# Kernel optimization log

Measured on AMD Instinct MI355X. Metric: run time of the kernel, lower is better.

The kernel has to match this reference:

```python
import jax, jax.numpy as jnp
import numpy as np

B, L, D, A = 64, 512, 512, 512  # batch, seq_len, word_embed_size, alignment_size


def setup_inputs() -> dict:
    key = jax.random.key(0)
    k1, k2, k3 = jax.random.split(key, 3)
    premises = jax.random.normal(k1, (B, L, D), dtype=jnp.float32)
    hypotheses = jax.random.normal(k2, (B, L, D), dtype=jnp.float32)
    W_F = jax.random.uniform(k3, (D, A), dtype=jnp.float32, minval=-1.0, maxval=1.0)
    return {"premises": premises, "hypotheses": hypotheses, "W_F": W_F}


def reference(premises, hypotheses, W_F):
    # tanh-projected cross attention (decomposable-attention align step)
    F_p = jnp.tanh(jnp.einsum('bpd,da->bpa', premises, W_F))    # [B, Lp, A]
    F_h = jnp.tanh(jnp.einsum('bhd,da->bha', hypotheses, W_F))  # [B, Lh, A]
    eijs = jnp.einsum('bpa,bha->bph', F_p, F_h)                 # [B, Lp, Lh] (unscaled)
    attn = jax.nn.softmax(eijs, axis=-1)                        # softmax over hypothesis axis
    betas = jnp.einsum('bph,bhd->bpd', attn, hypotheses)        # [B, Lp, D]
    alphas = jnp.einsum('bph,bpd->bhd', attn, premises)         # [B, Lh, D] (transpose(attn) @ P)
    return betas, alphas
```

## Files before the change

kernel.cpp:

```cpp
#include <hip/hip_runtime.h>
#include <hip/hip_fp16.h>


#define NB 64
#define NL 512
#define ND 512
#define BATCH_ELEMS (512 * 512)
#define TOT_ELEMS   ((size_t)NB * NL * ND)

typedef _Float16 h8 __attribute__((ext_vector_type(8)));
typedef float f4 __attribute__((ext_vector_type(4)));

__device__ __forceinline__ int swz(int row, int chunk) {
    return (row << 5) + ((chunk ^ (((row >> 1) ^ (row >> 4)) & 3)) << 3);
}

__device__ __forceinline__ float fast_tanh(float x) {
    float e = __expf(2.0f * x);
    return 1.0f - 2.0f / (e + 1.0f);
}

template <bool WITH_LO>
__global__ __launch_bounds__(256) void transpose_f16_kernel(
    const float* __restrict__ src, _Float16* __restrict__ dstH,
    _Float16* __restrict__ dstL)
{
    __shared__ float tile[64 * 68];
    const size_t base = (size_t)blockIdx.z * BATCH_ELEMS;
    const int r0 = blockIdx.y * 64, c0 = blockIdx.x * 64;
    const int t = threadIdx.x;
    {
        int r = t >> 2, cq = (t & 3) * 16;
        const float* sp = src + base + (size_t)(r0 + r) * 512 + c0 + cq;
        *(float4*)&tile[r * 68 + cq]      = ((const float4*)sp)[0];
        *(float4*)&tile[r * 68 + cq + 4]  = ((const float4*)sp)[1];
        *(float4*)&tile[r * 68 + cq + 8]  = ((const float4*)sp)[2];
        *(float4*)&tile[r * 68 + cq + 12] = ((const float4*)sp)[3];
    }
    __syncthreads();
    {
        int c = t >> 2, rq = (t & 3) * 16;
        _Float16 hv[16], lv[16];
#pragma unroll
        for (int j = 0; j < 16; ++j) {
            float v = tile[(rq + j) * 68 + c];
            hv[j] = (_Float16)v;
            if (WITH_LO) lv[j] = (_Float16)(v - (float)hv[j]);
        }
        _Float16* dp = dstH + base + (size_t)(c0 + c) * 512 + r0 + rq;
        *(h8*)dp = *(h8*)&hv[0];
        *(h8*)(dp + 8) = *(h8*)&hv[8];
        if (WITH_LO) {
            _Float16* dl = dstL + base + (size_t)(c0 + c) * 512 + r0 + rq;
            *(h8*)dl = *(h8*)&lv[0];
            *(h8*)(dl + 8) = *(h8*)&lv[8];
        }
    }
}

__global__ __launch_bounds__(256) void transpose_hp_kernel(
    const float* __restrict__ H, const float* __restrict__ P,
    _Float16* __restrict__ HT, _Float16* __restrict__ PT)
{
    __shared__ float tile[64 * 68];
    const int z = blockIdx.z;
    const float* src = (z < NB) ? H : P;
    _Float16* dst = (z < NB) ? HT : PT;
    const size_t base = (size_t)(z < NB ? z : z - NB) * BATCH_ELEMS;
    const int r0 = blockIdx.y * 64, c0 = blockIdx.x * 64;
    const int t = threadIdx.x;
    {
        int r = t >> 2, cq = (t & 3) * 16;
        const float* sp = src + base + (size_t)(r0 + r) * 512 + c0 + cq;
        *(float4*)&tile[r * 68 + cq]      = ((const float4*)sp)[0];
        *(float4*)&tile[r * 68 + cq + 4]  = ((const float4*)sp)[1];
        *(float4*)&tile[r * 68 + cq + 8]  = ((const float4*)sp)[2];
        *(float4*)&tile[r * 68 + cq + 12] = ((const float4*)sp)[3];
    }
    __syncthreads();
    {
        int c = t >> 2, rq = (t & 3) * 16;
        _Float16 hv[16];
#pragma unroll
        for (int j = 0; j < 16; ++j) hv[j] = (_Float16)tile[(rq + j) * 68 + c];
        _Float16* dp = dst + base + (size_t)(c0 + c) * 512 + r0 + rq;
        *(h8*)dp = *(h8*)&hv[0];
        *(h8*)(dp + 8) = *(h8*)&hv[8];
    }
}

__global__ __launch_bounds__(256) void proj_tanh_kernel(
    const float* __restrict__ P, const float* __restrict__ H,
    const _Float16* __restrict__ WTH, const _Float16* __restrict__ WTL,
    _Float16* __restrict__ Fout)
{
    __shared__ __align__(16) _Float16 AsH[2][128 * 32];
    __shared__ __align__(16) _Float16 BsH[2][128 * 32], BsL[2][128 * 32];

    const int z = blockIdx.z;
    const float* X = z ? H : P;
    _Float16* F = Fout + (size_t)z * TOT_ELEMS;
    const int r0 = blockIdx.x * 128;
    const int n0 = blockIdx.y * 128;

    const int t = threadIdx.x;
    const int lane = t & 63, w = t >> 6;
    const int q = lane >> 4, c = lane & 15;
    const int wm = w >> 1, wn = w & 1;

    f4 acc[4][4] = {};

    const int ar = t >> 1, akq = (t & 1) << 4;
    const int br = t >> 1, bcp = (t & 1) << 1;

    const float* apg = X + (size_t)(r0 + ar) * 512 + akq;
    const _Float16* bhg = WTH + (size_t)(n0 + br) * 512 + bcp * 8;
    const _Float16* blg = WTL + (size_t)(n0 + br) * 512 + bcp * 8;

    float av[2][16];
    h8 bh0[2], bh1[2], bl0[2], bl1[2];

    auto LOAD = [&](int k0, int s) {
        *(float4*)&av[s][0]  = ((const float4*)(apg + k0))[0];
        *(float4*)&av[s][4]  = ((const float4*)(apg + k0))[1];
        *(float4*)&av[s][8]  = ((const float4*)(apg + k0))[2];
        *(float4*)&av[s][12] = ((const float4*)(apg + k0))[3];
        bh0[s] = ((const h8*)(bhg + k0))[0];
        bh1[s] = ((const h8*)(bhg + k0))[1];
        bl0[s] = ((const h8*)(blg + k0))[0];
        bl1[s] = ((const h8*)(blg + k0))[1];
    };
    auto STAGE = [&](int s, int pp) {
        _Float16* asd = &AsH[pp][0];
        _Float16* bhd = &BsH[pp][0];
        _Float16* bld = &BsL[pp][0];
        const int cbase = akq >> 3;
#pragma unroll
        for (int jj = 0; jj < 2; ++jj) {
            h8 hv;
#pragma unroll
            for (int i = 0; i < 8; ++i) hv[i] = (_Float16)av[s][jj * 8 + i];
            *(h8*)&asd[swz(ar, cbase + jj)] = hv;
        }
        *(h8*)&bhd[swz(br, bcp)]     = bh0[s];
        *(h8*)&bhd[swz(br, bcp + 1)] = bh1[s];
        *(h8*)&bld[swz(br, bcp)]     = bl0[s];
        *(h8*)&bld[swz(br, bcp + 1)] = bl1[s];
    };

    LOAD(0, 0);
    STAGE(0, 0);
    LOAD(32, 1);

    for (int ks = 0; ks < 16; ++ks) {
        __syncthreads();
        const int pp = ks & 1;
        if (ks + 2 < 16) LOAD((ks + 2) << 5, pp);

        const _Float16* ash = &AsH[pp][0];
        const _Float16* bhs = &BsH[pp][0];
        const _Float16* bls = &BsL[pp][0];
        h8 aH[4], bH[4], bL[4];
#pragma unroll
        for (int mi = 0; mi < 4; ++mi)
            aH[mi] = *(const h8*)&ash[swz(wm * 64 + mi * 16 + c, q)];
#pragma unroll
        for (int ni = 0; ni < 4; ++ni) {
            bH[ni] = *(const h8*)&bhs[swz(wn * 64 + ni * 16 + c, q)];
            bL[ni] = *(const h8*)&bls[swz(wn * 64 + ni * 16 + c, q)];
        }
#pragma unroll
        for (int mi = 0; mi < 4; ++mi)
#pragma unroll
            for (int ni = 0; ni < 4; ++ni) {
                acc[mi][ni] = __builtin_amdgcn_mfma_f32_16x16x32_f16(aH[mi], bH[ni], acc[mi][ni], 0, 0, 0);
                acc[mi][ni] = __builtin_amdgcn_mfma_f32_16x16x32_f16(aH[mi], bL[ni], acc[mi][ni], 0, 0, 0);
            }
        if (ks + 1 < 16) STAGE((ks + 1) & 1, pp ^ 1);
    }

#pragma unroll
    for (int mi = 0; mi < 4; ++mi)
#pragma unroll
        for (int ni = 0; ni < 4; ++ni) {
            int col = n0 + wn * 64 + ni * 16 + c;
            int rowb = r0 + wm * 64 + mi * 16 + q * 4;
#pragma unroll
            for (int r = 0; r < 4; ++r)
                F[(size_t)(rowb + r) * 512 + col] = (_Float16)fast_tanh(acc[mi][ni][r]);
        }
}

__global__ __launch_bounds__(256) void score_softmax_kernel(
    const _Float16* __restrict__ Fbase, _Float16* __restrict__ attn)
{
    __shared__ __align__(16) _Float16 As[2][64 * 32];
    __shared__ __align__(16) _Float16 Bs[2][512 * 32];
    __shared__ float redM[4 * 64], redS[4 * 64];

    const _Float16* Fp = Fbase;
    const _Float16* Fh = Fbase + TOT_ELEMS;
    const int b = blockIdx.y;
    const int p0 = blockIdx.x * 64;
    const size_t fb = (size_t)b * BATCH_ELEMS;

    const int t = threadIdx.x, lane = t & 63, w = t >> 6;
    const int q = lane >> 4, c = lane & 15;

    f4 acc[4][8] = {};

    const int arow = t >> 2, ach = t & 3;
    const _Float16* apg = Fp + fb + (size_t)(p0 + arow) * 512 + ach * 8;
    const _Float16* bpg = Fh + fb + (size_t)(t * 2) * 512;

    h8 areg, breg[2][4];

    auto LOAD = [&](int k0) {
        areg = *(const h8*)(apg + k0);
#pragma unroll
        for (int rr = 0; rr < 2; ++rr)
#pragma unroll
            for (int ch = 0; ch < 4; ++ch)
                breg[rr][ch] = *(const h8*)(bpg + (size_t)rr * 512 + k0 + ch * 8);
    };
    auto STAGE = [&](int pp) {
        *(h8*)&As[pp][swz(arow, ach)] = areg;
#pragma unroll
        for (int rr = 0; rr < 2; ++rr)
#pragma unroll
            for (int ch = 0; ch < 4; ++ch)
                *(h8*)&Bs[pp][swz(t * 2 + rr, ch)] = breg[rr][ch];
    };

    LOAD(0);
    STAGE(0);

    int pp = 0;
    for (int k0 = 0; k0 < 512; k0 += 32) {
        __syncthreads();
        const bool more = (k0 + 32) < 512;
        if (more) LOAD(k0 + 32);

        h8 a[4], bb[8];
#pragma unroll
        for (int mt = 0; mt < 4; ++mt) a[mt] = *(const h8*)&As[pp][swz(mt * 16 + c, q)];
#pragma unroll
        for (int nt = 0; nt < 8; ++nt) bb[nt] = *(const h8*)&Bs[pp][swz(w * 128 + nt * 16 + c, q)];
#pragma unroll
        for (int mt = 0; mt < 4; ++mt)
#pragma unroll
            for (int nt = 0; nt < 8; ++nt)
                acc[mt][nt] = __builtin_amdgcn_mfma_f32_16x16x32_f16(a[mt], bb[nt], acc[mt][nt], 0, 0, 0);
        if (more) STAGE(pp ^ 1);
        pp ^= 1;
    }

    float rmax[4][4];
#pragma unroll
    for (int mt = 0; mt < 4; ++mt)
#pragma unroll
        for (int r = 0; r < 4; ++r) {
            float m = acc[mt][0][r];
#pragma unroll
            for (int nt = 1; nt < 8; ++nt) m = fmaxf(m, acc[mt][nt][r]);
            rmax[mt][r] = m;
        }
#pragma unroll
    for (int s = 1; s < 16; s <<= 1)
#pragma unroll
        for (int mt = 0; mt < 4; ++mt)
#pragma unroll
            for (int r = 0; r < 4; ++r)
                rmax[mt][r] = fmaxf(rmax[mt][r], __shfl_xor(rmax[mt][r], s, 64));
    if (c == 0)
#pragma unroll
        for (int mt = 0; mt < 4; ++mt)
#pragma unroll
            for (int r = 0; r < 4; ++r)
                redM[w * 64 + mt * 16 + q * 4 + r] = rmax[mt][r];
    __syncthreads();

    float gmax[4][4];
#pragma unroll
    for (int mt = 0; mt < 4; ++mt)
#pragma unroll
        for (int r = 0; r < 4; ++r) {
            int row = mt * 16 + q * 4 + r;
            float m = redM[row];
#pragma unroll
            for (int w4 = 1; w4 < 4; ++w4) m = fmaxf(m, redM[w4 * 64 + row]);
            gmax[mt][r] = m;
        }

    float rsum[4][4] = {};
#pragma unroll
    for (int mt = 0; mt < 4; ++mt)
#pragma unroll
        for (int nt = 0; nt < 8; ++nt)
#pragma unroll
            for (int r = 0; r < 4; ++r) {
                float e = __expf(acc[mt][nt][r] - gmax[mt][r]);
                acc[mt][nt][r] = e;
                rsum[mt][r] += e;
            }
#pragma unroll
    for (int s = 1; s < 16; s <<= 1)
#pragma unroll
        for (int mt = 0; mt < 4; ++mt)
#pragma unroll
            for (int r = 0; r < 4; ++r)
                rsum[mt][r] += __shfl_xor(rsum[mt][r], s, 64);
    if (c == 0)
#pragma unroll
        for (int mt = 0; mt < 4; ++mt)
#pragma unroll
            for (int r = 0; r < 4; ++r)
                redS[w * 64 + mt * 16 + q * 4 + r] = rsum[mt][r];
    __syncthreads();

    float inv[4][4];
#pragma unroll
    for (int mt = 0; mt < 4; ++mt)
#pragma unroll
        for (int r = 0; r < 4; ++r) {
            int row = mt * 16 + q * 4 + r;
            float s = redS[row] + redS[64 + row] + redS[128 + row] + redS[192 + row];
            inv[mt][r] = 1.0f / s;
        }

#pragma unroll
    for (int mt = 0; mt < 4; ++mt)
#pragma unroll
        for (int nt = 0; nt < 8; ++nt) {
            int col = w * 128 + nt * 16 + c;
#pragma unroll
            for (int r = 0; r < 4; ++r) {
                int row = p0 + mt * 16 + q * 4 + r;
                attn[fb + (size_t)row * 512 + col] = (_Float16)(acc[mt][nt][r] * inv[mt][r]);
            }
        }
}

__global__ __launch_bounds__(256) void out_gemm_kernel(
    const _Float16* __restrict__ Amat, const _Float16* __restrict__ HT,
    const _Float16* __restrict__ PT, float* __restrict__ out)
{
    __shared__ __align__(16) _Float16 As[2][128 * 32];
    __shared__ __align__(16) _Float16 Bs[2][128 * 32];

    const int zz = blockIdx.z;
    const bool transA = zz >= NB;
    const int b = transA ? zz - NB : zz;
    const _Float16* BT = transA ? PT : HT;
    float* Cout = transA ? out + TOT_ELEMS : out;

    const int bn = blockIdx.x * 128, bm = blockIdx.y * 128;
    const size_t base = (size_t)b * BATCH_ELEMS;

    const int t = threadIdx.x, lane = t & 63, w = t >> 6;
    const int q = lane >> 4, c = lane & 15;
    const int wm = w >> 1, wn = w & 1;

    f4 acc[4][4] = {};

    const int row2 = t >> 1, cp2 = (t & 1) * 2;
    const int kk = t >> 3, m0 = (t & 7) * 16;
    const _Float16* apg_d = Amat + base + (size_t)(bm + row2) * 512 + cp2 * 8;
    const _Float16* apg_t = Amat + base + (size_t)kk * 512 + bm + m0;
    const _Float16* bpg   = BT + base + (size_t)(bn + row2) * 512 + cp2 * 8;

    h8 a0[2], a1[2], b0[2], b1[2];

    auto LOAD = [&](int k0, int s) {
        if (!transA) {
            a0[s] = ((const h8*)(apg_d + k0))[0];
            a1[s] = ((const h8*)(apg_d + k0))[1];
        } else {
            a0[s] = ((const h8*)(apg_t + (size_t)k0 * 512))[0];
            a1[s] = ((const h8*)(apg_t + (size_t)k0 * 512))[1];
        }
        b0[s] = ((const h8*)(bpg + k0))[0];
        b1[s] = ((const h8*)(bpg + k0))[1];
    };
    auto STAGE = [&](int s, int pp) {
        if (!transA) {
            *(h8*)&As[pp][swz(row2, cp2)]     = a0[s];
            *(h8*)&As[pp][swz(row2, cp2 + 1)] = a1[s];
        } else {
#pragma unroll
            for (int j = 0; j < 8; ++j) {
                As[pp][swz(m0 + j, kk >> 3) + (kk & 7)]     = a0[s][j];
                As[pp][swz(m0 + 8 + j, kk >> 3) + (kk & 7)] = a1[s][j];
            }
        }
        *(h8*)&Bs[pp][swz(row2, cp2)]     = b0[s];
        *(h8*)&Bs[pp][swz(row2, cp2 + 1)] = b1[s];
    };

    LOAD(0, 0);
    STAGE(0, 0);
    LOAD(32, 1);

    for (int ks = 0; ks < 16; ++ks) {
        __syncthreads();
        const int pp = ks & 1;
        if (ks + 2 < 16) LOAD((ks + 2) << 5, pp);

        h8 a[4], bb[4];
#pragma unroll
        for (int mi = 0; mi < 4; ++mi) a[mi] = *(const h8*)&As[pp][swz(wm * 64 + mi * 16 + c, q)];
#pragma unroll
        for (int ni = 0; ni < 4; ++ni) bb[ni] = *(const h8*)&Bs[pp][swz(wn * 64 + ni * 16 + c, q)];
#pragma unroll
        for (int mi = 0; mi < 4; ++mi)
#pragma unroll
            for (int ni = 0; ni < 4; ++ni)
                acc[mi][ni] = __builtin_amdgcn_mfma_f32_16x16x32_f16(a[mi], bb[ni], acc[mi][ni], 0, 0, 0);
        if (ks + 1 < 16) STAGE((ks + 1) & 1, pp ^ 1);
    }

#pragma unroll
    for (int mi = 0; mi < 4; ++mi)
#pragma unroll
        for (int ni = 0; ni < 4; ++ni) {
            int col = bn + wn * 64 + ni * 16 + c;
            int rowb = bm + wm * 64 + mi * 16 + q * 4;
#pragma unroll
            for (int r = 0; r < 4; ++r)
                Cout[base + (size_t)(rowb + r) * 512 + col] = acc[mi][ni][r];
        }
}

extern "C" void kernel_launch(void* const* d_in, const int* in_sizes, int n_in,
                              void* d_out, int out_size, void* d_ws, size_t ws_size,
                              hipStream_t stream) {
    const float* P = (const float*)d_in[0];
    const float* H = (const float*)d_in[1];
    const float* W = (const float*)d_in[2];
    float* out = (float*)d_out;

    _Float16* ws16 = (_Float16*)d_ws;
    _Float16* F    = ws16;
    _Float16* PT   = ws16;
    _Float16* HT   = ws16 + TOT_ELEMS;
    _Float16* attn = ws16 + 2 * TOT_ELEMS;
    _Float16* WTH  = attn;
    _Float16* WTL  = attn + BATCH_ELEMS;

    transpose_f16_kernel<true><<<dim3(8, 8, 1), 256, 0, stream>>>(W, WTH, WTL);
    proj_tanh_kernel<<<dim3(256, 4, 2), 256, 0, stream>>>(P, H, WTH, WTL, F);
    score_softmax_kernel<<<dim3(8, NB), 256, 0, stream>>>(F, attn);
    transpose_hp_kernel<<<dim3(8, 8, 2 * NB), 256, 0, stream>>>(H, P, HT, PT);
    out_gemm_kernel<<<dim3(4, 4, 2 * NB), 256, 0, stream>>>(attn, HT, PT, out);
}
```

Before: 506.9 us.

## Use direct global-to-LDS loads in GEMM kernels and pre-convert inputs to fp16

Replaces the register-staged double-buffer loads in the projection, score and output GEMM kernels with global_load_lds direct-to-LDS copies. The swizzle is applied on the source address so the existing LDS layout is kept. To make the projection input fp16 for these loads, a new conversion kernel writes P and H as fp16 into the output buffer as scratch before the main pipeline. The aim is to cut VGPR staging and LDS write instructions. The cost is an extra pass over the inputs and a different synchronisation pattern per k-step.

Result: no change. 503.9 us (-0.6%).

```diff
diff --git a/kernel.cpp b/kernel.cpp
--- a/kernel.cpp
+++ b/kernel.cpp
@@ -15,9 +15,33 @@
     return (row << 5) + ((chunk ^ (((row >> 1) ^ (row >> 4)) & 3)) << 3);
 }
 
+__device__ __forceinline__ void gld16(const _Float16* g, _Float16* l) {
+    __builtin_amdgcn_global_load_lds(
+        (const __attribute__((address_space(1))) void*)g,
+        (__attribute__((address_space(3))) void*)l, 16, 0, 0);
+}
+
 __device__ __forceinline__ float fast_tanh(float x) {
     float e = __expf(2.0f * x);
     return 1.0f - 2.0f / (e + 1.0f);
+}
+
+__global__ __launch_bounds__(256) void conv16_kernel(
+    const float* __restrict__ P, const float* __restrict__ H,
+    _Float16* __restrict__ X16)
+{
+    const int z = blockIdx.z;
+    const float* src = z ? H : P;
+    _Float16* dst = X16 + (size_t)z * TOT_ELEMS;
+    size_t i = ((size_t)blockIdx.x * 256 + threadIdx.x) * 8;
+    float4 v0 = ((const float4*)(src + i))[0];
+    float4 v1 = ((const float4*)(src + i))[1];
+    h8 o;
+    o[0] = (_Float16)v0.x; o[1] = (_Float16)v0.y;
+    o[2] = (_Float16)v0.z; o[3] = (_Float16)v0.w;
+    o[4] = (_Float16)v1.x; o[5] = (_Float16)v1.y;
+    o[6] = (_Float16)v1.z; o[7] = (_Float16)v1.w;
+    *(h8*)(dst + i) = o;
 }
 
 template <bool WITH_LO>
@@ -90,7 +114,7 @@
 }
 
 __global__ __launch_bounds__(256) void proj_tanh_kernel(
-    const float* __restrict__ P, const float* __restrict__ H,
+    const _Float16* __restrict__ X16,
     const _Float16* __restrict__ WTH, const _Float16* __restrict__ WTL,
     _Float16* __restrict__ Fout)
 {
@@ -98,76 +122,53 @@
     __shared__ __align__(16) _Float16 BsH[2][128 * 32], BsL[2][128 * 32];
 
     const int z = blockIdx.z;
-    const float* X = z ? H : P;
+    const _Float16* X = X16 + (size_t)z * TOT_ELEMS;
     _Float16* F = Fout + (size_t)z * TOT_ELEMS;
     const int r0 = blockIdx.x * 128;
     const int n0 = blockIdx.y * 128;
 
     const int t = threadIdx.x;
-    const int lane = t & 63, w = t >> 6;
+    const int lane = t & 63, w4 = t >> 6;
     const int q = lane >> 4, c = lane & 15;
-    const int wm = w >> 1, wn = w & 1;
+    const int wm = w4 >> 1, wn = w4 & 1;
 
     f4 acc[4][4] = {};
 
-    const int ar = t >> 1, akq = (t & 1) << 4;
-    const int br = t >> 1, bcp = (t & 1) << 1;
-
-    const float* apg = X + (size_t)(r0 + ar) * 512 + akq;
-    const _Float16* bhg = WTH + (size_t)(n0 + br) * 512 + bcp * 8;
-    const _Float16* blg = WTL + (size_t)(n0 + br) * 512 + bcp * 8;
-
-    float av[2][16];
-    h8 bh0[2], bh1[2], bl0[2], bl1[2];
-
-    auto LOAD = [&](int k0, int s) {
-        *(float4*)&av[s][0]  = ((const float4*)(apg + k0))[0];
-        *(float4*)&av[s][4]  = ((const float4*)(apg + k0))[1];
-        *(float4*)&av[s][8]  = ((const float4*)(apg + k0))[2];
-        *(float4*)&av[s][12] = ((const float4*)(apg + k0))[3];
-        bh0[s] = ((const h8*)(bhg + k0))[0];
-        bh1[s] = ((const h8*)(bhg + k0))[1];
-        bl0[s] = ((const h8*)(blg + k0))[0];
-        bl1[s] = ((const h8*)(blg + k0))[1];
-    };
-    auto STAGE = [&](int s, int pp) {
-        _Float16* asd = &AsH[pp][0];
-        _Float16* bhd = &BsH[pp][0];
-        _Float16* bld = &BsL[pp][0];
-        const int cbase = akq >> 3;
-#pragma unroll
-        for (int jj = 0; jj < 2; ++jj) {
-            h8 hv;
-#pragma unroll
-            for (int i = 0; i < 8; ++i) hv[i] = (_Float16)av[s][jj * 8 + i];
-            *(h8*)&asd[swz(ar, cbase + jj)] = hv;
-        }
-        *(h8*)&bhd[swz(br, bcp)]     = bh0[s];
-        *(h8*)&bhd[swz(br, bcp + 1)] = bh1[s];
-        *(h8*)&bld[swz(br, bcp)]     = bl0[s];
-        *(h8*)&bld[swz(br, bcp + 1)] = bl1[s];
-    };
-
-    LOAD(0, 0);
+    const int lr = w4 * 16 + (lane >> 2);
+    const int sb = ((lr >> 1) ^ (lr >> 4)) & 3;
+    const int ch = ((lane & 3) ^ sb) * 8;
+    const _Float16* sA0 = X + (size_t)(r0 + lr) * 512 + ch;
+    const _Float16* sA1 = sA0 + (size_t)64 * 512;
+    const _Float16* sH0 = WTH + (size_t)(n0 + lr) * 512 + ch;
+    const _Float16* sH1 = sH0 + (size_t)64 * 512;
+    const _Float16* sL0 = WTL + (size_t)(n0 + lr) * 512 + ch;
+    const _Float16* sL1 = sL0 + (size_t)64 * 512;
+    const int d0 = (w4 * 16) * 32, d1 = (64 + w4 * 16) * 32;
+
+    auto STAGE = [&](int pp, int k0) {
+        gld16(sA0 + k0, &AsH[pp][d0]);
+        gld16(sA1 + k0, &AsH[pp][d1]);
+        gld16(sH0 + k0, &BsH[pp][d0]);
+        gld16(sH1 + k0, &BsH[pp][d1]);
+        gld16(sL0 + k0, &BsL[pp][d0]);
+        gld16(sL1 + k0, &BsL[pp][d1]);
+    };
+
     STAGE(0, 0);
-    LOAD(32, 1);
+    __syncthreads();
 
     for (int ks = 0; ks < 16; ++ks) {
-        __syncthreads();
         const int pp = ks & 1;
-        if (ks + 2 < 16) LOAD((ks + 2) << 5, pp);
-
-        const _Float16* ash = &AsH[pp][0];
-        const _Float16* bhs = &BsH[pp][0];
-        const _Float16* bls = &BsL[pp][0];
+        if (ks + 1 < 16) STAGE(pp ^ 1, (ks + 1) << 5);
+
         h8 aH[4], bH[4], bL[4];
 #pragma unroll
         for (int mi = 0; mi < 4; ++mi)
-            aH[mi] = *(const h8*)&ash[swz(wm * 64 + mi * 16 + c, q)];
+            aH[mi] = *(const h8*)&AsH[pp][swz(wm * 64 + mi * 16 + c, q)];
 #pragma unroll
         for (int ni = 0; ni < 4; ++ni) {
-            bH[ni] = *(const h8*)&bhs[swz(wn * 64 + ni * 16 + c, q)];
-            bL[ni] = *(const h8*)&bls[swz(wn * 64 + ni * 16 + c, q)];
+            bH[ni] = *(const h8*)&BsH[pp][swz(wn * 64 + ni * 16 + c, q)];
+            bL[ni] = *(const h8*)&BsL[pp][swz(wn * 64 + ni * 16 + c, q)];
         }
 #pragma unroll
         for (int mi = 0; mi < 4; ++mi)
@@ -176,7 +177,7 @@
                 acc[mi][ni] = __builtin_amdgcn_mfma_f32_16x16x32_f16(aH[mi], bH[ni], acc[mi][ni], 0, 0, 0);
                 acc[mi][ni] = __builtin_amdgcn_mfma_f32_16x16x32_f16(aH[mi], bL[ni], acc[mi][ni], 0, 0, 0);
             }
-        if (ks + 1 < 16) STAGE((ks + 1) & 1, pp ^ 1);
+        __syncthreads();
     }
 
 #pragma unroll
@@ -209,37 +210,26 @@
 
     f4 acc[4][8] = {};
 
-    const int arow = t >> 2, ach = t & 3;
-    const _Float16* apg = Fp + fb + (size_t)(p0 + arow) * 512 + ach * 8;
-    const _Float16* bpg = Fh + fb + (size_t)(t * 2) * 512;
-
-    h8 areg, breg[2][4];
-
-    auto LOAD = [&](int k0) {
-        areg = *(const h8*)(apg + k0);
-#pragma unroll
-        for (int rr = 0; rr < 2; ++rr)
-#pragma unroll
-            for (int ch = 0; ch < 4; ++ch)
-                breg[rr][ch] = *(const h8*)(bpg + (size_t)rr * 512 + k0 + ch * 8);
-    };
-    auto STAGE = [&](int pp) {
-        *(h8*)&As[pp][swz(arow, ach)] = areg;
-#pragma unroll
-        for (int rr = 0; rr < 2; ++rr)
-#pragma unroll
-            for (int ch = 0; ch < 4; ++ch)
-                *(h8*)&Bs[pp][swz(t * 2 + rr, ch)] = breg[rr][ch];
-    };
-
-    LOAD(0);
-    STAGE(0);
-
-    int pp = 0;
-    for (int k0 = 0; k0 < 512; k0 += 32) {
-        __syncthreads();
-        const bool more = (k0 + 32) < 512;
-        if (more) LOAD(k0 + 32);
+    const int lr = w * 16 + (lane >> 2);
+    const int sb = ((lr >> 1) ^ (lr >> 4)) & 3;
+    const int ch = ((lane & 3) ^ sb) * 8;
+    const _Float16* sA  = Fp + fb + (size_t)(p0 + lr) * 512 + ch;
+    const _Float16* sB0 = Fh + fb + (size_t)lr * 512 + ch;
+    const int dA = (w * 16) * 32;
+
+    auto STAGE = [&](int pp, int k0) {
+        gld16(sA + k0, &As[pp][dA]);
+#pragma unroll
+        for (int i = 0; i < 8; ++i)
+            gld16(sB0 + (size_t)i * 64 * 512 + k0, &Bs[pp][(i * 64 + w * 16) * 32]);
+    };
+
+    STAGE(0, 0);
+    __syncthreads();
+
+    for (int ks = 0; ks < 16; ++ks) {
+        const int pp = ks & 1;
+        if (ks + 1 < 16) STAGE(pp ^ 1, (ks + 1) << 5);
 
         h8 a[4], bb[8];
 #pragma unroll
@@ -251,8 +241,7 @@
 #pragma unroll
             for (int nt = 0; nt < 8; ++nt)
                 acc[mt][nt] = __builtin_amdgcn_mfma_f32_16x16x32_f16(a[mt], bb[nt], acc[mt][nt], 0, 0, 0);
-        if (more) STAGE(pp ^ 1);
-        pp ^= 1;
+        __syncthreads();
     }
 
     float rmax[4][4];
@@ -288,7 +277,7 @@
             int row = mt * 16 + q * 4 + r;
             float m = redM[row];
 #pragma unroll
-            for (int w4 = 1; w4 < 4; ++w4) m = fmaxf(m, redM[w4 * 64 + row]);
+            for (int w4i = 1; w4i < 4; ++w4i) m = fmaxf(m, redM[w4i * 64 + row]);
             gmax[mt][r] = m;
         }
 
@@ -357,54 +346,63 @@
     const int bn = blockIdx.x * 128, bm = blockIdx.y * 128;
     const size_t base = (size_t)b * BATCH_ELEMS;
 
-    const int t = threadIdx.x, lane = t & 63, w = t >> 6;
+    const int t = threadIdx.x, lane = t & 63, w4 = t >> 6;
     const int q = lane >> 4, c = lane & 15;
-    const int wm = w >> 1, wn = w & 1;
+    const int wm = w4 >> 1, wn = w4 & 1;
 
     f4 acc[4][4] = {};
 
-    const int row2 = t >> 1, cp2 = (t & 1) * 2;
+    const int lr = w4 * 16 + (lane >> 2);
+    const int sb = ((lr >> 1) ^ (lr >> 4)) & 3;
+    const int ch = ((lane & 3) ^ sb) * 8;
+    const _Float16* sA0 = Amat + base + (size_t)(bm + lr) * 512 + ch;
+    const _Float16* sA1 = sA0 + (size_t)64 * 512;
+    const _Float16* sB0 = BT + base + (size_t)(bn + lr) * 512 + ch;
+    const _Float16* sB1 = sB0 + (size_t)64 * 512;
+    const int d0 = (w4 * 16) * 32, d1 = (64 + w4 * 16) * 32;
+
     const int kk = t >> 3, m0 = (t & 7) * 16;
-    const _Float16* apg_d = Amat + base + (size_t)(bm + row2) * 512 + cp2 * 8;
     const _Float16* apg_t = Amat + base + (size_t)kk * 512 + bm + m0;
-    const _Float16* bpg   = BT + base + (size_t)(bn + row2) * 512 + cp2 * 8;
-
-    h8 a0[2], a1[2], b0[2], b1[2];
-
-    auto LOAD = [&](int k0, int s) {
-        if (!transA) {
-            a0[s] = ((const h8*)(apg_d + k0))[0];
-            a1[s] = ((const h8*)(apg_d + k0))[1];
-        } else {
-            a0[s] = ((const h8*)(apg_t + (size_t)k0 * 512))[0];
-            a1[s] = ((const h8*)(apg_t + (size_t)k0 * 512))[1];
-        }
-        b0[s] = ((const h8*)(bpg + k0))[0];
-        b1[s] = ((const h8*)(bpg + k0))[1];
-    };
-    auto STAGE = [&](int s, int pp) {
-        if (!transA) {
-            *(h8*)&As[pp][swz(row2, cp2)]     = a0[s];
-            *(h8*)&As[pp][swz(row2, cp2 + 1)] = a1[s];
-        } else {
-#pragma unroll
-            for (int j = 0; j < 8; ++j) {
-                As[pp][swz(m0 + j, kk >> 3) + (kk & 7)]     = a0[s][j];
-                As[pp][swz(m0 + 8 + j, kk >> 3) + (kk & 7)] = a1[s][j];
-            }
-        }
-        *(h8*)&Bs[pp][swz(row2, cp2)]     = b0[s];
-        *(h8*)&Bs[pp][swz(row2, cp2 + 1)] = b1[s];
-    };
-
-    LOAD(0, 0);
-    STAGE(0, 0);
-    LOAD(32, 1);
+    h8 a0, a1;
+
+    auto STAGE_B = [&](int pp, int k0) {
+        gld16(sB0 + k0, &Bs[pp][d0]);
+        gld16(sB1 + k0, &Bs[pp][d1]);
+    };
+    auto STAGE_A_DIRECT = [&](int pp, int k0) {
+        gld16(sA0 + k0, &As[pp][d0]);
+        gld16(sA1 + k0, &As[pp][d1]);
+    };
+    auto LOAD_A_T = [&](int k0) {
+        a0 = ((const h8*)(apg_t + (size_t)k0 * 512))[0];
+        a1 = ((const h8*)(apg_t + (size_t)k0 * 512))[1];
+    };
+    auto STAGE_A_T = [&](int pp) {
+#pragma unroll
+        for (int j = 0; j < 8; ++j) {
+            As[pp][swz(m0 + j, kk >> 3) + (kk & 7)]     = a0[j];
+            As[pp][swz(m0 + 8 + j, kk >> 3) + (kk & 7)] = a1[j];
+        }
+    };
+
+    STAGE_B(0, 0);
+    if (!transA) {
+        STAGE_A_DIRECT(0, 0);
+    } else {
+        LOAD_A_T(0);
+        STAGE_A_T(0);
+    }
+    __syncthreads();
 
     for (int ks = 0; ks < 16; ++ks) {
-        __syncthreads();
         const int pp = ks & 1;
-        if (ks + 2 < 16) LOAD((ks + 2) << 5, pp);
+        const bool more = (ks + 1) < 16;
+        const int k0n = (ks + 1) << 5;
+        if (more) {
+            STAGE_B(pp ^ 1, k0n);
+            if (!transA) STAGE_A_DIRECT(pp ^ 1, k0n);
+            else LOAD_A_T(k0n);
+        }
 
         h8 a[4], bb[4];
 #pragma unroll
@@ -416,7 +414,8 @@
 #pragma unroll
             for (int ni = 0; ni < 4; ++ni)
                 acc[mi][ni] = __builtin_amdgcn_mfma_f32_16x16x32_f16(a[mi], bb[ni], acc[mi][ni], 0, 0, 0);
-        if (ks + 1 < 16) STAGE((ks + 1) & 1, pp ^ 1);
+        if (more && transA) STAGE_A_T(pp ^ 1);
+        __syncthreads();
     }
 
 #pragma unroll
@@ -446,9 +445,11 @@
     _Float16* attn = ws16 + 2 * TOT_ELEMS;
     _Float16* WTH  = attn;
     _Float16* WTL  = attn + BATCH_ELEMS;
-
+    _Float16* X16  = (_Float16*)d_out;
+
+    conv16_kernel<<<dim3(8192, 1, 2), 256, 0, stream>>>(P, H, X16);
     transpose_f16_kernel<true><<<dim3(8, 8, 1), 256, 0, stream>>>(W, WTH, WTL);
-    proj_tanh_kernel<<<dim3(256, 4, 2), 256, 0, stream>>>(P, H, WTH, WTL, F);
+    proj_tanh_kernel<<<dim3(256, 4, 2), 256, 0, stream>>>(X16, WTH, WTL, F);
     score_softmax_kernel<<<dim3(8, NB), 256, 0, stream>>>(F, attn);
     transpose_hp_kernel<<<dim3(8, 8, 2 * NB), 256, 0, stream>>>(H, P, HT, PT);
     out_gemm_kernel<<<dim3(4, 4, 2 * NB), 256, 0, stream>>>(attn, HT, PT, out);
```
